# Performance work log

Hardware: AMD Instinct MI355X
Metric: run time of the kernel (lower is better)

The kernel has to match this reference:

```python
import jax, jax.numpy as jnp
import numpy as np

N_CELLS = 196608  # 12 * 4**7 (HEALPix zoom 7)
NH = 9            # cell + 8 neighbors
F_IN = 64
F_OUT = 64


def setup_inputs() -> dict:
    key = jax.random.key(0)
    k1, k2, k3 = jax.random.split(key, 3)
    x = jax.random.normal(k1, (1, 1, 1, N_CELLS, F_IN), dtype=jnp.float32)
    adjc = jax.random.randint(k2, (N_CELLS, NH), 0, N_CELLS, dtype=jnp.int32)
    W = jax.random.normal(k3, (NH * F_IN, F_OUT), dtype=jnp.float32) * (1.0 / np.sqrt(NH * F_IN))
    return {"x": x, "adjc": adjc, "W": W}


def reference(x, adjc, W):
    # get_nh: gather neighborhood features along the cell axis.
    # x: [B, V, T, N, F], adjc: [N, NH] -> xnh: [B, V, T, N, NH, F]
    xnh = jnp.take(x, adjc, axis=3)
    B, V, T, N = xnh.shape[:4]
    # LinearLayer: flatten (NH, F) -> NH*F, dense projection to F_OUT (no bias)
    xf = xnh.reshape(B, V, T, N, NH * x.shape[-1])
    out = jnp.einsum('bvtnk,ko->bvtno', xf, W)  # [B, V, T, N, F_OUT]
    return out
```

## Files before the change

### kernel.cpp

```cpp
#include <hip/hip_runtime.h>
#include <hip/hip_bf16.h>
#include <stdint.h>

#define N_CELLS 196608
#define NH 9
#define F 64
#define K_TOT (NH * F)
#define K_STEPS (K_TOT / 32)

typedef __attribute__((ext_vector_type(8))) short bf16x8;
typedef __attribute__((ext_vector_type(4))) float f32x4;

__device__ inline unsigned short f2bf(float f) {
    union { float f; uint32_t u; } v; v.f = f;
    uint32_t u = v.u;
    uint32_t r = u + 0x7FFFu + ((u >> 16) & 1u);
    return (unsigned short)(r >> 16);
}

__global__ __launch_bounds__(256) void convert_x_kernel(
        const float* __restrict__ x, unsigned short* __restrict__ xb) {
    size_t i = (size_t)blockIdx.x * blockDim.x + threadIdx.x;
    const f32x4* p = reinterpret_cast<const f32x4*>(x);
    f32x4 a = p[i * 2], b = p[i * 2 + 1];
    unsigned short tmp[8];
    #pragma unroll
    for (int j = 0; j < 4; ++j) { tmp[j] = f2bf(a[j]); tmp[4 + j] = f2bf(b[j]); }
    *reinterpret_cast<bf16x8*>(xb + i * 8) = *reinterpret_cast<const bf16x8*>(tmp);
}

__global__ __launch_bounds__(256) void convert_w_kernel(
        const float* __restrict__ W, unsigned short* __restrict__ wb) {
    int tid = blockIdx.x * blockDim.x + threadIdx.x;
    int l = tid & 63;
    int frag = tid >> 6;
    int kk = frag >> 2, t = frag & 3;
    int k0 = kk * 32 + (l >> 4) * 8;
    int o  = t * 16 + (l & 15);
    unsigned short tmp[8];
    #pragma unroll
    for (int j = 0; j < 8; ++j) tmp[j] = f2bf(W[(size_t)(k0 + j) * F + o]);
    *reinterpret_cast<bf16x8*>(wb + (size_t)tid * 8) =
        *reinterpret_cast<const bf16x8*>(tmp);
}

template <bool XB>
__global__ __launch_bounds__(256) void fused_gather_gemm(
        const float* __restrict__ x32, const unsigned short* __restrict__ xb,
        const int* __restrict__ adjc, const unsigned short* __restrict__ wb,
        float* __restrict__ out) {
    const int wave = threadIdx.x >> 6;
    const int lane = threadIdx.x & 63;
    const int lo = lane & 15, hi = lane >> 4;
    const int cellbase = blockIdx.x * 64 + wave * 16;
    const int cell = cellbase + lo;

    f32x4 acc[4] = {f32x4{0,0,0,0}, f32x4{0,0,0,0}, f32x4{0,0,0,0}, f32x4{0,0,0,0}};
    const size_t adj_base = (size_t)cell * NH;

    #pragma unroll
    for (int j = 0; j < NH; ++j) {
        const int idx = adjc[adj_base + j];
        #pragma unroll
        for (int h = 0; h < 2; ++h) {
            bf16x8 a;
            if (XB) {
                a = *reinterpret_cast<const bf16x8*>(
                        xb + (size_t)idx * F + h * 32 + hi * 8);
            } else {
                const float* ap = x32 + (size_t)idx * F + h * 32 + hi * 8;
                f32x4 f0 = *reinterpret_cast<const f32x4*>(ap);
                f32x4 f1 = *reinterpret_cast<const f32x4*>(ap + 4);
                unsigned short tmp[8];
                #pragma unroll
                for (int q = 0; q < 4; ++q) { tmp[q] = f2bf(f0[q]); tmp[4+q] = f2bf(f1[q]); }
                a = *reinterpret_cast<const bf16x8*>(tmp);
            }
            const int kk = j * 2 + h;
            #pragma unroll
            for (int t = 0; t < 4; ++t) {
                bf16x8 b = *reinterpret_cast<const bf16x8*>(
                        wb + ((size_t)(kk * 4 + t) * 64 + lane) * 8);
                acc[t] = __builtin_amdgcn_mfma_f32_16x16x32_bf16(a, b, acc[t], 0, 0, 0);
            }
        }
    }

    #pragma unroll
    for (int t = 0; t < 4; ++t) {
        #pragma unroll
        for (int r = 0; r < 4; ++r) {
            int row = cellbase + hi * 4 + r;
            out[(size_t)row * F + t * 16 + lo] = acc[t][r];
        }
    }
}

__global__ void naive_kernel(const float* __restrict__ x,
                             const int* __restrict__ adjc,
                             const float* __restrict__ W,
                             float* __restrict__ out) {
    int n = blockIdx.x;
    int o = threadIdx.x;
    float acc = 0.f;
    for (int j = 0; j < NH; ++j) {
        int idx = adjc[(size_t)n * NH + j];
        for (int f = 0; f < F; ++f)
            acc += x[(size_t)idx * F + f] * W[(size_t)(j * F + f) * F + o];
    }
    out[(size_t)n * F + o] = acc;
}

extern "C" void kernel_launch(void* const* d_in, const int* in_sizes, int n_in,
                              void* d_out, int out_size, void* d_ws, size_t ws_size,
                              hipStream_t stream) {
    const float* x    = (const float*)d_in[0];
    const int*   adjc = (const int*)d_in[1];
    const float* W    = (const float*)d_in[2];
    float* out = (float*)d_out;

    const size_t need_x = (size_t)N_CELLS * F * sizeof(unsigned short);
    const size_t need_w = (size_t)K_TOT * F * sizeof(unsigned short);

    if (ws_size >= need_x + need_w) {
        unsigned short* xb = (unsigned short*)d_ws;
        unsigned short* wb = (unsigned short*)((char*)d_ws + need_x);
        convert_x_kernel<<<(N_CELLS * F / 8) / 256, 256, 0, stream>>>(x, xb);
        convert_w_kernel<<<(K_STEPS * 4 * 64) / 256, 256, 0, stream>>>(W, wb);
        fused_gather_gemm<true><<<N_CELLS / 64, 256, 0, stream>>>(x, xb, adjc, wb, out);
    } else if (ws_size >= need_w) {
        unsigned short* wb = (unsigned short*)d_ws;
        convert_w_kernel<<<(K_STEPS * 4 * 64) / 256, 256, 0, stream>>>(W, wb);
        fused_gather_gemm<false><<<N_CELLS / 64, 256, 0, stream>>>(x, nullptr, adjc, wb, out);
    } else {
        naive_kernel<<<N_CELLS, F, 0, stream>>>(x, adjc, W, out);
    }
}
```

Before: 74.81 us.

## Process four 16-cell tiles per wave with prefetched gathers and shared W fragments

```diff
diff --git a/kernel.cpp b/kernel.cpp
--- a/kernel.cpp
+++ b/kernel.cpp
@@ -45,55 +45,89 @@
 }
 
 template <bool XB>
-__global__ __launch_bounds__(256) void fused_gather_gemm(
+__global__ __launch_bounds__(256) void fused_gather_gemm_v2(
         const float* __restrict__ x32, const unsigned short* __restrict__ xb,
         const int* __restrict__ adjc, const unsigned short* __restrict__ wb,
         float* __restrict__ out) {
     const int wave = threadIdx.x >> 6;
     const int lane = threadIdx.x & 63;
     const int lo = lane & 15, hi = lane >> 4;
-    const int cellbase = blockIdx.x * 64 + wave * 16;
-    const int cell = cellbase + lo;
+    const int cellbase = blockIdx.x * 256 + wave * 64;
 
-    f32x4 acc[4] = {f32x4{0,0,0,0}, f32x4{0,0,0,0}, f32x4{0,0,0,0}, f32x4{0,0,0,0}};
-    const size_t adj_base = (size_t)cell * NH;
+    int idx[4][NH];
+    #pragma unroll
+    for (int m = 0; m < 4; ++m) {
+        const int* ap = adjc + (size_t)(cellbase + m * 16 + lo) * NH;
+        #pragma unroll
+        for (int j = 0; j < NH; ++j) idx[m][j] = ap[j];
+    }
+
+    f32x4 acc[4][4];
+    #pragma unroll
+    for (int m = 0; m < 4; ++m)
+        #pragma unroll
+        for (int t = 0; t < 4; ++t) acc[m][t] = f32x4{0.f, 0.f, 0.f, 0.f};
+
+    auto loadA = [&](int m, int j, int h) -> bf16x8 {
+        if (XB) {
+            return *reinterpret_cast<const bf16x8*>(
+                    xb + (size_t)idx[m][j] * F + h * 32 + hi * 8);
+        } else {
+            const float* ap = x32 + (size_t)idx[m][j] * F + h * 32 + hi * 8;
+            f32x4 f0 = *reinterpret_cast<const f32x4*>(ap);
+            f32x4 f1 = *reinterpret_cast<const f32x4*>(ap + 4);
+            unsigned short tmp[8];
+            #pragma unroll
+            for (int q = 0; q < 4; ++q) { tmp[q] = f2bf(f0[q]); tmp[4+q] = f2bf(f1[q]); }
+            return *reinterpret_cast<const bf16x8*>(tmp);
+        }
+    };
+
+    bf16x8 aC[4][2];
+    #pragma unroll
+    for (int m = 0; m < 4; ++m)
+        #pragma unroll
+        for (int h = 0; h < 2; ++h) aC[m][h] = loadA(m, 0, h);
 
     #pragma unroll
     for (int j = 0; j < NH; ++j) {
-        const int idx = adjc[adj_base + j];
+        bf16x8 aN[4][2];
+        if (j + 1 < NH) {
+            #pragma unroll
+            for (int m = 0; m < 4; ++m)
+                #pragma unroll
+                for (int h = 0; h < 2; ++h) aN[m][h] = loadA(m, j + 1, h);
+        }
         #pragma unroll
         for (int h = 0; h < 2; ++h) {
-            bf16x8 a;
-            if (XB) {
-                a = *reinterpret_cast<const bf16x8*>(
-                        xb + (size_t)idx * F + h * 32 + hi * 8);
-            } else {
-                const float* ap = x32 + (size_t)idx * F + h * 32 + hi * 8;
-                f32x4 f0 = *reinterpret_cast<const f32x4*>(ap);
-                f32x4 f1 = *reinterpret_cast<const f32x4*>(ap + 4);
-                unsigned short tmp[8];
-                #pragma unroll
-                for (int q = 0; q < 4; ++q) { tmp[q] = f2bf(f0[q]); tmp[4+q] = f2bf(f1[q]); }
-                a = *reinterpret_cast<const bf16x8*>(tmp);
-            }
             const int kk = j * 2 + h;
             #pragma unroll
             for (int t = 0; t < 4; ++t) {
                 bf16x8 b = *reinterpret_cast<const bf16x8*>(
                         wb + ((size_t)(kk * 4 + t) * 64 + lane) * 8);
-                acc[t] = __builtin_amdgcn_mfma_f32_16x16x32_bf16(a, b, acc[t], 0, 0, 0);
+                #pragma unroll
+                for (int m = 0; m < 4; ++m)
+                    acc[m][t] = __builtin_amdgcn_mfma_f32_16x16x32_bf16(
+                            aC[m][h], b, acc[m][t], 0, 0, 0);
             }
+        }
+        if (j + 1 < NH) {
+            #pragma unroll
+            for (int m = 0; m < 4; ++m)
+                #pragma unroll
+                for (int h = 0; h < 2; ++h) aC[m][h] = aN[m][h];
         }
     }
 
     #pragma unroll
-    for (int t = 0; t < 4; ++t) {
+    for (int m = 0; m < 4; ++m)
         #pragma unroll
-        for (int r = 0; r < 4; ++r) {
-            int row = cellbase + hi * 4 + r;
-            out[(size_t)row * F + t * 16 + lo] = acc[t][r];
-        }
-    }
+        for (int t = 0; t < 4; ++t)
+            #pragma unroll
+            for (int r = 0; r < 4; ++r) {
+                int row = cellbase + m * 16 + hi * 4 + r;
+                out[(size_t)row * F + t * 16 + lo] = acc[m][t][r];
+            }
 }
 
 __global__ void naive_kernel(const float* __restrict__ x,
@@ -127,11 +161,13 @@
         unsigned short* wb = (unsigned short*)((char*)d_ws + need_x);
         convert_x_kernel<<<(N_CELLS * F / 8) / 256, 256, 0, stream>>>(x, xb);
         convert_w_kernel<<<(K_STEPS * 4 * 64) / 256, 256, 0, stream>>>(W, wb);
-        fused_gather_gemm<true><<<N_CELLS / 64, 256, 0, stream>>>(x, xb, adjc, wb, out);
+        fused_gather_gemm_v2<true><<<N_CELLS / 256, 256, 0, stream>>>(
+                x, xb, adjc, wb, out);
     } else if (ws_size >= need_w) {
         unsigned short* wb = (unsigned short*)d_ws;
         convert_w_kernel<<<(K_STEPS * 4 * 64) / 256, 256, 0, stream>>>(W, wb);
-        fused_gather_gemm<false><<<N_CELLS / 64, 256, 0, stream>>>(x, nullptr, adjc, wb, out);
+        fused_gather_gemm_v2<false><<<N_CELLS / 256, 256, 0, stream>>>(
+                x, nullptr, adjc, wb, out);
     } else {
         naive_kernel<<<N_CELLS, F, 0, stream>>>(x, adjc, W, out);
     }
```

Result: faster. 71.33 us (-4.6%).
